# Kernel tuning notes

Hardware: AMD Instinct MI355X
Metric: run time of the kernel (lower is better)

## Reference

```python
import jax, jax.numpy as jnp
import numpy as np

D, K, STRIDE, PADDING = 5, 3, 1, 2
B, CIN, COUT, H, W = 32, 128, 256, 56, 56


def _conv(x, w, stride, padding):
    return jax.lax.conv_general_dilated(
        x, w, window_strides=(stride, stride),
        padding=[(padding, padding), (padding, padding)],
        dimension_numbers=("NCHW", "OIHW", "NCHW"))


def setup_inputs() -> dict:
    key = jax.random.key(0)
    k1, k2, k3 = jax.random.split(key, 3)
    x = jax.random.normal(k1, (B, CIN, H, W), dtype=jnp.float32)
    # kaiming-uniform-ish core init
    fan_in = CIN * K * K
    bound = float(np.sqrt(6.0 / fan_in))
    core = jax.random.uniform(k2, (COUT, CIN, K, K), dtype=jnp.float32,
                              minval=-bound, maxval=bound)
    periphery = jax.random.uniform(k3, (D * D - K * K,), dtype=jnp.float32,
                                   minval=-0.1, maxval=0.1)
    thresh = jnp.ones((COUT,), jnp.float32) * 0.1
    scale = jnp.array([10.0], jnp.float32)
    return {"x": x, "core": core, "periphery": periphery,
            "thresh": thresh, "scale": scale}


def reference(x, core, periphery, thresh, scale):
    pad = (D - K) // 2  # offset of the KxK core inside the DxD window
    # Dense core conv: embed KxK core at the center of a DxD kernel so core
    # and periphery share the same output grid (padding=PADDING for DxD).
    core_full = jnp.pad(core, ((0, 0), (0, 0), (pad, pad), (pad, pad)))
    core_out = _conv(x, core_full, STRIDE, PADDING)  # [B, COUT, Ho, Wo]

    # Periphery: one shared scalar per off-core offset, shared across all
    # in/out channels -> sum input over channels, conv with a 1x1-channel
    # DxD stencil whose core region is zero.
    periph_mask = np.ones((D, D), dtype=bool)
    periph_mask[pad:pad + K, pad:pad + K] = False
    periph_idx = np.flatnonzero(periph_mask)  # row-major off-core offsets
    pk = jnp.zeros((D * D,), x.dtype).at[periph_idx].set(periphery)
    pk = pk.reshape(1, 1, D, D)
    xs = jnp.sum(x, axis=1, keepdims=True)  # [B,1,H,W]
    periph_out = _conv(xs, pk, STRIDE, PADDING)  # [B,1,Ho,Wo]

    # Per-out-channel threshold/scale gating: periphery term is switched on
    # where the core response exceeds the channel threshold (soft gate).
    gate = jax.nn.sigmoid(scale[0] * (core_out - thresh[None, :, None, None]))
    return core_out + gate * periph_out
```

## Files before the change

### kernel.cpp

```cpp
#include <hip/hip_runtime.h>

typedef __attribute__((__ext_vector_type__(8))) _Float16 f16x8;
typedef __attribute__((__ext_vector_type__(4))) float f32x4;
typedef __attribute__((__ext_vector_type__(4))) int i32x4;

#define HW 56
#define HW2 3136
#define CIN 128
#define COUT 256
#define NB 32
#define NPIX 100352
#define PH 58

static __device__ __forceinline__ unsigned short f2h(float f) {
  _Float16 h = (_Float16)f;
  return __builtin_bit_cast(unsigned short, h);
}

#define GLD_LDS16(g, l)                                          \
  __builtin_amdgcn_global_load_lds(                              \
      (const __attribute__((address_space(1))) void*)(g),        \
      (__attribute__((address_space(3))) void*)(l), 16, 0, 0)

__global__ __launch_bounds__(256) void prep_x(const float* __restrict__ x,
                                              unsigned short* __restrict__ xp,
                                              float* __restrict__ xs) {
  if (blockIdx.x >= NB * HW) {
    int t = (blockIdx.x - NB * HW) * 256 + threadIdx.x;
    int ck = t & 15;
    int pi = t >> 4;
    int b = pi / 228, r = pi - b * 228;
    int h, w;
    if (r < 58) { h = 0; w = r; }
    else if (r < 116) { h = 57; w = r - 58; }
    else { int q = r - 116; h = 1 + (q >> 1); w = (q & 1) * 57; }
    size_t off = (((size_t)(b * PH + h) * PH + w) << 8) + (ck << 4);
    *reinterpret_cast<i32x4*>((char*)xp + off) = (i32x4){0, 0, 0, 0};
    return;
  }
  __shared__ float tile[CIN * 57];
  const int bh = blockIdx.x;
  const float* src = x + (size_t)(bh / HW) * CIN * HW2 + (size_t)(bh % HW) * HW;
  for (int idx = threadIdx.x; idx < CIN * HW; idx += 256) {
    int c = idx / HW, w = idx - c * HW;
    tile[c * 57 + w] = src[(size_t)c * HW2 + w];
  }
  __syncthreads();
  unsigned short* dst =
      xp + (((size_t)(bh / HW) * PH + (bh % HW) + 1) * PH + 1) * CIN;
  for (int idx = threadIdx.x; idx < HW * (CIN / 2); idx += 256) {
    int w = idx >> 6;
    int c = (idx & 63) << 1;
    unsigned lo = f2h(tile[c * 57 + w]);
    unsigned hi = f2h(tile[(c + 1) * 57 + w]);
    *reinterpret_cast<unsigned*>(&dst[w * CIN + c]) = lo | (hi << 16);
  }
  if (threadIdx.x < HW) {
    float s = 0.f;
    for (int c = 0; c < CIN; ++c) s += tile[c * 57 + threadIdx.x];
    xs[(size_t)bh * HW + threadIdx.x] = s;
  }
}

__global__ __launch_bounds__(256) void prep_w(const float* __restrict__ core,
                                              unsigned short* __restrict__ w_t) {
  int i = blockIdx.x * 256 + threadIdx.x;
  int c = i & 127;
  int p = (i >> 7) % 9;
  int m = i / (9 * 128);
  w_t[i] = f2h(core[(size_t)(m * CIN + c) * 9 + p]);
}

__global__ __launch_bounds__(256) void periph_k(const float* __restrict__ xs,
                                                const float* __restrict__ per,
                                                float* __restrict__ po) {
  int n = blockIdx.x * 256 + threadIdx.x;
  int b = n / HW2, r = n - b * HW2;
  int ho = r / HW, wo = r - ho * HW;
  const float* xb = xs + (size_t)b * HW2;
  const int pdy[16] = {0,0,0,0,0,1,1,2,2,3,3,4,4,4,4,4};
  const int pdx[16] = {0,1,2,3,4,0,4,0,4,0,4,0,1,2,3,4};
  float acc = 0.f;
#pragma unroll
  for (int t = 0; t < 16; ++t) {
    int h = ho + pdy[t] - 2, w = wo + pdx[t] - 2;
    if ((unsigned)h < HW && (unsigned)w < HW) acc += per[t] * xb[h * HW + w];
  }
  po[n] = acc;
}

__global__ __launch_bounds__(256, 3) void gemm_k(const unsigned short* __restrict__ xp,
                                                 const unsigned short* __restrict__ w_t,
                                                 const float* __restrict__ po,
                                                 const float* __restrict__ thresh,
                                                 const float* __restrict__ scale,
                                                 float* __restrict__ out) {
  __shared__ __align__(16) char sMem[2 * 24576];

  const int tid = threadIdx.x;
  const int lane = tid & 63;
  const int wid = tid >> 6;
  const int wm = wid >> 1;
  const int wn = wid & 1;

  const int bid = blockIdx.x;
  const int n0 = ((bid & 7) * 98 + (bid >> 3)) << 7;

  const int l4 = lane >> 2;
  const int ls = lane & 3;
  const int sw = (ls ^ ((l4 >> 1) & 3)) << 4;
  const char* xpc = (const char*)xp;
  const char* wtc = (const char*)w_t;
  const int aSrc0 = (wid * 16 + l4) * 2304 + sw;
  int bSrc[2];
#pragma unroll
  for (int k = 0; k < 2; ++k) {
    int n = n0 + wid * 16 + k * 64 + l4;
    int b = n / HW2, rr = n - b * HW2;
    int h = rr / HW, w = rr - h * HW;
    bSrc[k] = ((b * PH + h + 1) * PH + (w + 1)) * 256 + sw;
  }

  const int rowA0 = wm * 128 + (lane & 15);
  const int aro0 = rowA0 * 64 + ((((lane >> 4) ^ (rowA0 >> 1)) & 3) << 4);
  const int rowB0 = wn * 64 + (lane & 15);
  const int bro0 = 16384 + rowB0 * 64 + ((((lane >> 4) ^ (rowB0 >> 1)) & 3) << 4);

  auto STAGE = [&](int buf, int t) {
    const int p = t >> 2;
    const int cq = t & 3;
    const int dy = p / 3 - 1, dx = p - (p / 3) * 3 - 1;
    const int offA = (p << 8) + (cq << 6);
    const int offB = ((dy * PH + dx) << 8) + (cq << 6);
    char* base = sMem + buf * 24576;
#pragma unroll
    for (int k = 0; k < 4; ++k)
      GLD_LDS16(wtc + aSrc0 + k * 147456 + offA, base + (wid + 4 * k) * 1024);
#pragma unroll
    for (int k = 0; k < 2; ++k)
      GLD_LDS16(xpc + bSrc[k] + offB, base + 16384 + (wid + 4 * k) * 1024);
  };

  f32x4 acc[8][4] = {};

  STAGE(0, 0);
  __syncthreads();

  for (int t = 0; t < 36; ++t) {
    const char* base = sMem + (t & 1) * 24576;
    __builtin_amdgcn_s_barrier();
    if (t < 35) {
      STAGE((t + 1) & 1, t + 1);
      asm volatile("s_waitcnt vmcnt(6)" ::: "memory");
    } else {
      asm volatile("s_waitcnt vmcnt(0)" ::: "memory");
    }
    __builtin_amdgcn_s_barrier();

    f16x8 bfr[4];
#pragma unroll
    for (int j = 0; j < 4; ++j)
      bfr[j] = *reinterpret_cast<const f16x8*>(base + bro0 + j * 1024);
#pragma unroll
    for (int i = 0; i < 8; ++i) {
      f16x8 af = *reinterpret_cast<const f16x8*>(base + aro0 + i * 1024);
      __builtin_amdgcn_s_setprio(1);
#pragma unroll
      for (int j = 0; j < 4; ++j)
        acc[i][j] = __builtin_amdgcn_mfma_f32_16x16x32_f16(af, bfr[j], acc[i][j], 0, 0, 0);
      __builtin_amdgcn_s_setprio(0);
    }
  }

  const float sc = scale[0];
#pragma unroll
  for (int j = 0; j < 4; ++j) {
    int n = n0 + wn * 64 + j * 16 + (lane & 15);
    int b = n / HW2;
    int r = n - b * HW2;
    float pv = po[n];
    float* op = out + (size_t)b * (COUT * HW2) + r;
#pragma unroll
    for (int i = 0; i < 8; ++i) {
      int cl = wm * 128 + i * 16 + ((lane >> 4) << 2);
      f32x4 th = *reinterpret_cast<const f32x4*>(&thresh[cl]);
#pragma unroll
      for (int q = 0; q < 4; ++q) {
        float cv = acc[i][j][q];
        float g = 1.f / (1.f + __expf(-sc * (cv - th[q])));
        op[(size_t)(cl + q) * HW2] = cv + g * pv;
      }
    }
  }
}

extern "C" void kernel_launch(void* const* d_in, const int* in_sizes, int n_in,
                              void* d_out, int out_size, void* d_ws, size_t ws_size,
                              hipStream_t stream) {
  (void)in_sizes; (void)n_in; (void)out_size; (void)ws_size;
  const float* x      = (const float*)d_in[0];
  const float* core   = (const float*)d_in[1];
  const float* per    = (const float*)d_in[2];
  const float* thresh = (const float*)d_in[3];
  const float* scale  = (const float*)d_in[4];
  float* out = (float*)d_out;

  char* ws = (char*)d_ws;
  unsigned short* xp  = (unsigned short*)ws;
  unsigned short* w_t = (unsigned short*)(ws + 27557888);
  float* xs           = (float*)(ws + 28147712);
  float* po           = (float*)(ws + 28549120);

  prep_x<<<NB * HW + 456, 256, 0, stream>>>(x, xp, xs);
  prep_w<<<(COUT * 9 * CIN) / 256, 256, 0, stream>>>(core, w_t);
  periph_k<<<NPIX / 256, 256, 0, stream>>>(xs, per, po);
  gemm_k<<<NPIX / 128, 256, 0, stream>>>(xp, w_t, po, thresh, scale, out);
}
```

Baseline: 120.8 us.

## Drop LDS staging in conv GEMM; load fragments directly from global with register double-buffering

The implicit-GEMM kernel no longer stages A/B tiles through LDS with global_load_lds and barriers. Each wave now loads its MFMA operand fragments straight from global memory into registers and double-buffers them across K steps. The block tile shrinks from 256x128 to 256x64 pixels, which doubles the grid. This removes LDS traffic and barrier syncs, but each block's A tile is no longer shared across waves, so global/L2 traffic rises and data reuse is lower.

Result: slower. 261.8 us (+116.6%).

```diff
diff --git a/kernel.cpp b/kernel.cpp
--- a/kernel.cpp
+++ b/kernel.cpp
@@ -16,11 +16,6 @@
   _Float16 h = (_Float16)f;
   return __builtin_bit_cast(unsigned short, h);
 }
-
-#define GLD_LDS16(g, l)                                          \
-  __builtin_amdgcn_global_load_lds(                              \
-      (const __attribute__((address_space(1))) void*)(g),        \
-      (__attribute__((address_space(3))) void*)(l), 16, 0, 0)
 
 __global__ __launch_bounds__(256) void prep_x(const float* __restrict__ x,
                                               unsigned short* __restrict__ xp,
@@ -95,94 +90,80 @@
                                                  const float* __restrict__ thresh,
                                                  const float* __restrict__ scale,
                                                  float* __restrict__ out) {
-  __shared__ __align__(16) char sMem[2 * 24576];
-
   const int tid = threadIdx.x;
   const int lane = tid & 63;
-  const int wid = tid >> 6;
-  const int wm = wid >> 1;
-  const int wn = wid & 1;
+  const int wm = tid >> 6;
 
   const int bid = blockIdx.x;
-  const int n0 = ((bid & 7) * 98 + (bid >> 3)) << 7;
+  const int n0 = ((bid & 7) * 196 + (bid >> 3)) << 6;
 
-  const int l4 = lane >> 2;
-  const int ls = lane & 3;
-  const int sw = (ls ^ ((l4 >> 1) & 3)) << 4;
   const char* xpc = (const char*)xp;
   const char* wtc = (const char*)w_t;
-  const int aSrc0 = (wid * 16 + l4) * 2304 + sw;
-  int bSrc[2];
+
+  int aOff[4], bOff[4];
 #pragma unroll
-  for (int k = 0; k < 2; ++k) {
-    int n = n0 + wid * 16 + k * 64 + l4;
+  for (int i = 0; i < 4; ++i)
+    aOff[i] = (wm * 64 + i * 16 + (lane & 15)) * 2304 + ((lane >> 4) << 4);
+#pragma unroll
+  for (int j = 0; j < 4; ++j) {
+    int n = n0 + j * 16 + (lane & 15);
     int b = n / HW2, rr = n - b * HW2;
     int h = rr / HW, w = rr - h * HW;
-    bSrc[k] = ((b * PH + h + 1) * PH + (w + 1)) * 256 + sw;
+    bOff[j] = ((b * PH + h + 1) * PH + (w + 1)) * 256 + ((lane >> 4) << 4);
   }
 
-  const int rowA0 = wm * 128 + (lane & 15);
-  const int aro0 = rowA0 * 64 + ((((lane >> 4) ^ (rowA0 >> 1)) & 3) << 4);
-  const int rowB0 = wn * 64 + (lane & 15);
-  const int bro0 = 16384 + rowB0 * 64 + ((((lane >> 4) ^ (rowB0 >> 1)) & 3) << 4);
-
-  auto STAGE = [&](int buf, int t) {
-    const int p = t >> 2;
-    const int cq = t & 3;
-    const int dy = p / 3 - 1, dx = p - (p / 3) * 3 - 1;
-    const int offA = (p << 8) + (cq << 6);
-    const int offB = ((dy * PH + dx) << 8) + (cq << 6);
-    char* base = sMem + buf * 24576;
-#pragma unroll
-    for (int k = 0; k < 4; ++k)
-      GLD_LDS16(wtc + aSrc0 + k * 147456 + offA, base + (wid + 4 * k) * 1024);
-#pragma unroll
-    for (int k = 0; k < 2; ++k)
-      GLD_LDS16(xpc + bSrc[k] + offB, base + 16384 + (wid + 4 * k) * 1024);
+  auto toffA = [](int t) { return ((t >> 2) << 8) + ((t & 3) << 6); };
+  auto toffB = [](int t) {
+    int p = t >> 2;
+    int dy = p / 3 - 1, dx = p - (p / 3) * 3 - 1;
+    return ((dy * PH + dx) << 8) + ((t & 3) << 6);
   };
 
-  f32x4 acc[8][4] = {};
+#define LOADT(A, B, t)                                                    \
+  {                                                                       \
+    const int ta_ = toffA(t), tb_ = toffB(t);                             \
+    _Pragma("unroll") for (int i_ = 0; i_ < 4; ++i_)                      \
+        A[i_] = *reinterpret_cast<const f16x8*>(wtc + aOff[i_] + ta_);    \
+    _Pragma("unroll") for (int j_ = 0; j_ < 4; ++j_)                      \
+        B[j_] = *reinterpret_cast<const f16x8*>(xpc + bOff[j_] + tb_);    \
+  }
 
-  STAGE(0, 0);
-  __syncthreads();
+  f32x4 acc[4][4] = {};
+  f16x8 pa[4], pb[4], qa[4], qb[4];
 
-  for (int t = 0; t < 36; ++t) {
-    const char* base = sMem + (t & 1) * 24576;
-    __builtin_amdgcn_s_barrier();
-    if (t < 35) {
-      STAGE((t + 1) & 1, t + 1);
-      asm volatile("s_waitcnt vmcnt(6)" ::: "memory");
-    } else {
-      asm volatile("s_waitcnt vmcnt(0)" ::: "memory");
-    }
-    __builtin_amdgcn_s_barrier();
-
-    f16x8 bfr[4];
+  LOADT(pa, pb, 0)
+  for (int tt = 0; tt < 18; ++tt) {
+    const int t = 2 * tt;
+    LOADT(qa, qb, t + 1)
+    __builtin_amdgcn_s_setprio(1);
 #pragma unroll
-    for (int j = 0; j < 4; ++j)
-      bfr[j] = *reinterpret_cast<const f16x8*>(base + bro0 + j * 1024);
-#pragma unroll
-    for (int i = 0; i < 8; ++i) {
-      f16x8 af = *reinterpret_cast<const f16x8*>(base + aro0 + i * 1024);
-      __builtin_amdgcn_s_setprio(1);
+    for (int i = 0; i < 4; ++i)
 #pragma unroll
       for (int j = 0; j < 4; ++j)
-        acc[i][j] = __builtin_amdgcn_mfma_f32_16x16x32_f16(af, bfr[j], acc[i][j], 0, 0, 0);
-      __builtin_amdgcn_s_setprio(0);
-    }
+        acc[i][j] = __builtin_amdgcn_mfma_f32_16x16x32_f16(pa[i], pb[j], acc[i][j], 0, 0, 0);
+    __builtin_amdgcn_s_setprio(0);
+    if (t + 2 < 36) LOADT(pa, pb, t + 2)
+    __builtin_amdgcn_s_setprio(1);
+#pragma unroll
+    for (int i = 0; i < 4; ++i)
+#pragma unroll
+      for (int j = 0; j < 4; ++j)
+        acc[i][j] = __builtin_amdgcn_mfma_f32_16x16x32_f16(qa[i], qb[j], acc[i][j], 0, 0, 0);
+    __builtin_amdgcn_s_setprio(0);
   }
+#undef LOADT
 
   const float sc = scale[0];
 #pragma unroll
   for (int j = 0; j < 4; ++j) {
-    int n = n0 + wn * 64 + j * 16 + (lane & 15);
+    int n = n0 + j * 16 + (lane & 15);
     int b = n / HW2;
     int r = n - b * HW2;
     float pv = po[n];
     float* op = out + (size_t)b * (COUT * HW2) + r;
 #pragma unroll
-    for (int i = 0; i < 8; ++i) {
-      int cl = wm * 128 + i * 16 + ((lane >> 4) << 2);
+    for (int i = 0; i < 4; ++i) {
+      int cl = wm * 64 + i * 16 + ((lane >> 4) << 2);
       f32x4 th = *reinterpret_cast<const f32x4*>(&thresh[cl]);
 #pragma unroll
       for (int q = 0; q < 4; ++q) {
@@ -214,5 +195,5 @@
   prep_x<<<NB * HW + 456, 256, 0, stream>>>(x, xp, xs);
   prep_w<<<(COUT * 9 * CIN) / 256, 256, 0, stream>>>(core, w_t);
   periph_k<<<NPIX / 256, 256, 0, stream>>>(xs, per, po);
-  gemm_k<<<NPIX / 128, 256, 0, stream>>>(xp, w_t, po, thresh, scale, out);
+  gemm_k<<<NPIX / 64, 256, 0, stream>>>(xp, w_t, po, thresh, scale, out);
 }
```
